# Optimization experiments

Hardware: AMD Instinct MI355X
Metric: run time of the kernel (lower is better)

## Reference

```python
import jax, jax.numpy as jnp
import numpy as np

HEADS = 16
HEAD_DIM = 64
EMB = 1024
B, S = 4, 2048
SCALE = 1.0 / 8.0  # fixed constant in the original code
MASK_PENALTY = -50.0  # original adds -50 * upper_triangular, not -inf


def setup_inputs() -> dict:
    key = jax.random.key(0)
    ks = jax.random.split(key, 5)
    x = jax.random.normal(ks[0], (B, S, EMB), dtype=jnp.float32)
    Wq = jax.random.normal(ks[1], (EMB, HEADS * HEAD_DIM), dtype=jnp.float32) * 0.02
    Wk = jax.random.normal(ks[2], (EMB, HEADS * HEAD_DIM), dtype=jnp.float32) * 0.02
    Wv = jax.random.normal(ks[3], (EMB, HEADS * HEAD_DIM), dtype=jnp.float32) * 0.02
    Wr = jax.random.normal(ks[4], (HEADS * HEAD_DIM, EMB), dtype=jnp.float32) * 0.02
    return {"x": x, "Wq": Wq, "Wk": Wk, "Wv": Wv, "Wr": Wr}


def reference(x, Wq, Wk, Wv, Wr):
    b, s, _ = x.shape
    # project and split heads: [b, s, h, d]
    q = (x @ Wq).reshape(b, s, HEADS, HEAD_DIM)
    k = (x @ Wk).reshape(b, s, HEADS, HEAD_DIM)
    v = (x @ Wv).reshape(b, s, HEADS, HEAD_DIM)
    # scores: [b, h, s, s]
    scores = SCALE * jnp.einsum('bqhd,bkhd->bhqk', q, k)
    # causal additive mask: -50 on strictly-upper triangle (faithful to original)
    causal = jnp.triu(jnp.ones((s, s), dtype=x.dtype), k=1)
    scores = scores + MASK_PENALTY * causal
    attn = jax.nn.softmax(scores, axis=-1)
    out = jnp.einsum('bhqk,bkhd->bqhd', attn, v).reshape(b, s, HEADS * HEAD_DIM)
    return out @ Wr
```

## Files before the change

kernel.cpp:

```cpp
#include <hip/hip_runtime.h>

typedef _Float16 f16;
typedef _Float16 f16x8 __attribute__((ext_vector_type(8)));
typedef _Float16 f16x4 __attribute__((ext_vector_type(4)));
typedef float f32x4 __attribute__((ext_vector_type(4)));
typedef float f32x16 __attribute__((ext_vector_type(16)));

#define MFMA16(A, B, C) __builtin_amdgcn_mfma_f32_16x16x32_f16((A), (B), (C), 0, 0, 0)
#define MFMA32(A, B, C) __builtin_amdgcn_mfma_f32_32x32x16_f16((A), (B), (C), 0, 0, 0)
#define MFMA16K16(A, B, C) __builtin_amdgcn_mfma_f32_16x16x16f16((A), (B), (C), 0, 0, 0)

__device__ __forceinline__ void async16(void* lds, const void* gp) {
    __builtin_amdgcn_global_load_lds(
        (__attribute__((address_space(1))) void*)(gp),
        (__attribute__((address_space(3))) void*)(lds), 16, 0, 0);
}

__global__ __launch_bounds__(256) void k_convert(const float* __restrict__ in,
                                                 f16* __restrict__ out, int n) {
    int i = (blockIdx.x * 256 + threadIdx.x) * 4;
    if (i + 3 < n) {
        float4 v = *(const float4*)(in + i);
        f16x4 o = {(f16)v.x, (f16)v.y, (f16)v.z, (f16)v.w};
        *(f16x4*)(out + i) = o;
    }
}

__global__ __launch_bounds__(256) void k_transpose_w4(const float* __restrict__ Wq,
                                                      const float* __restrict__ Wk,
                                                      const float* __restrict__ Wv,
                                                      const float* __restrict__ Wr,
                                                      f16* __restrict__ Wqkvt,
                                                      f16* __restrict__ Wrt) {
    __shared__ float tile[32][33];
    int z = blockIdx.z;
    const float* W = (z == 0) ? Wq : (z == 1) ? Wk : (z == 2) ? Wv : Wr;
    f16* Wt = (z == 3) ? Wrt : Wqkvt + z * 1048576;
    int c0 = blockIdx.x * 32, r0 = blockIdx.y * 32;
    int tx = threadIdx.x, ty = threadIdx.y;
#pragma unroll
    for (int j = 0; j < 32; j += 8)
        tile[ty + j][tx] = W[(r0 + ty + j) * 1024 + c0 + tx];
    __syncthreads();
#pragma unroll
    for (int j = 0; j < 32; j += 8)
        Wt[(c0 + ty + j) * 1024 + r0 + tx] = (f16)tile[tx][ty + j];
}

__global__ __launch_bounds__(256) void k_transpose_v(const f16* __restrict__ QKV,
                                                     f16* __restrict__ Vt) {
    __shared__ f16 tile[32][33];
    int s0 = blockIdx.x * 32;
    int d0 = blockIdx.y * 32;
    int bh = blockIdx.z;
    int b = bh >> 4, h = bh & 15;
    int tx = threadIdx.x, ty = threadIdx.y;
#pragma unroll
    for (int j = 0; j < 32; j += 8)
        tile[ty + j][tx] = QKV[(b * 2048 + s0 + ty + j) * 3072 + 2048 + h * 64 + d0 + tx];
    __syncthreads();
#pragma unroll
    for (int j = 0; j < 32; j += 8)
        Vt[(bh * 64 + d0 + ty + j) * 2048 + s0 + tx] = tile[tx][ty + j];
}

template <bool OUT_F16>
__global__ __launch_bounds__(256, 4) void k_gemm_bt(const f16* __restrict__ A,
                                                    const f16* __restrict__ Bt,
                                                    void* __restrict__ Cv,
                                                    int M, int N, int K) {
    __shared__ f16 As[128][32];
    __shared__ f16 Bs[128][32];
    int t = threadIdx.x;
    int lane = t & 63, w = t >> 6;
    int wm = (w >> 1) * 64, wn = (w & 1) * 64;
    int m0 = blockIdx.y * 128, n0 = blockIdx.x * 128;
    int ln = lane & 31, kh = lane >> 5;
    int sw = (ln >> 1) & 3;

    int lin0 = w * 128 + lane, lin1 = lin0 + 64;
    int r0 = lin0 >> 2, c0 = (lin0 & 3) ^ ((r0 >> 1) & 3);
    int r1 = lin1 >> 2, c1 = (lin1 & 3) ^ ((r1 >> 1) & 3);
    const f16* gA0 = A + (size_t)(m0 + r0) * K + c0 * 8;
    const f16* gA1 = A + (size_t)(m0 + r1) * K + c1 * 8;
    const f16* gB0 = Bt + (size_t)(n0 + r0) * K + c0 * 8;
    const f16* gB1 = Bt + (size_t)(n0 + r1) * K + c1 * 8;
    f16* lA0 = &As[0][0] + w * 1024;
    f16* lB0 = &Bs[0][0] + w * 1024;

    f32x16 acc[2][2] = {};

    for (int k0 = 0; k0 < K; k0 += 32) {
        __syncthreads();
        async16(lA0, gA0 + k0);
        async16(lA0 + 512, gA1 + k0);
        async16(lB0, gB0 + k0);
        async16(lB0 + 512, gB1 + k0);
        __syncthreads();
#pragma unroll
        for (int kd = 0; kd < 2; kd++) {
            int c = kd * 2 + kh;
            f16x8 af[2], bf[2];
#pragma unroll
            for (int mt = 0; mt < 2; mt++)
                af[mt] = *(const f16x8*)&As[wm + mt * 32 + ln][(c ^ sw) * 8];
#pragma unroll
            for (int nt = 0; nt < 2; nt++)
                bf[nt] = *(const f16x8*)&Bs[wn + nt * 32 + ln][(c ^ sw) * 8];
#pragma unroll
            for (int mt = 0; mt < 2; mt++)
#pragma unroll
                for (int nt = 0; nt < 2; nt++)
                    acc[mt][nt] = MFMA32(af[mt], bf[nt], acc[mt][nt]);
        }
    }

#pragma unroll
    for (int mt = 0; mt < 2; mt++)
#pragma unroll
        for (int nt = 0; nt < 2; nt++)
#pragma unroll
            for (int r = 0; r < 16; r++) {
                int row = m0 + wm + mt * 32 + (r & 3) + 8 * (r >> 2) + 4 * kh;
                int col = n0 + wn + nt * 32 + ln;
                float v = acc[mt][nt][r];
                if (OUT_F16)
                    ((f16*)Cv)[(size_t)row * N + col] = (f16)v;
                else
                    ((float*)Cv)[(size_t)row * N + col] = v;
            }
}

__global__ __launch_bounds__(256, 2) void k_attn(const f16* __restrict__ QKV,
                                                 const f16* __restrict__ Vt,
                                                 f16* __restrict__ Ob) {
    __shared__ f16 Ks[64][72];
    __shared__ f16 Vs[64][72];
    int bh = blockIdx.x;
    int y = blockIdx.y;
    int qt = (y < 4) ? (7 - y) : (y - 4);
    int b = bh >> 4, h = bh & 15;
    int q0 = qt * 256;
    int t = threadIdx.x, lane = t & 63, wq = t >> 6;
    int ln = lane & 15, g = lane >> 4, g8 = g * 8, rg = g * 4;
    int qw = q0 + wq * 64;

    int kr0 = t >> 3, kc0 = (t & 7) * 8;
    int kr1 = (t + 256) >> 3, kc1 = (t & 7) * 8;
    const f16* Kbase = QKV + (size_t)b * 2048 * 3072 + 1024 + h * 64;
    const f16* Vbase = Vt + (size_t)bh * 64 * 2048;

    const float C_SCL = 0.18033688f;
    const float C_MSK = -72.134752f;
    f16x4 ones4 = {(f16)1.f, (f16)1.f, (f16)1.f, (f16)1.f};

    f16x8 bq[4][2];
#pragma unroll
    for (int nt = 0; nt < 4; nt++)
#pragma unroll
        for (int kd = 0; kd < 2; kd++)
            bq[nt][kd] = *(const f16x8*)(QKV +
                (size_t)(b * 2048 + qw + nt * 16 + ln) * 3072 + h * 64 + kd * 32 + g8);

    int4 rk0 = *(const int4*)(Kbase + (size_t)kr0 * 3072 + kc0);
    int4 rk1 = *(const int4*)(Kbase + (size_t)kr1 * 3072 + kc1);
    int4 rv0 = *(const int4*)(Vbase + (size_t)kr0 * 2048 + kc0);
    int4 rv1 = *(const int4*)(Vbase + (size_t)kr1 * 2048 + kc1);

    f32x4 oacc[4][4] = {};
    f32x4 osum[4] = {};
    int nk = 4 * qt + 4;

    for (int kt = 0; kt < nk; kt++) {
        int k0 = kt * 64;
        __syncthreads();
        *(int4*)&Ks[kr0][kc0] = rk0;
        *(int4*)&Ks[kr1][kc1] = rk1;
        *(int4*)&Vs[kr0][kc0] = rv0;
        *(int4*)&Vs[kr1][kc1] = rv1;
        if (kt + 1 < nk) {
            int kn = k0 + 64;
            rk0 = *(const int4*)(Kbase + (size_t)(kn + kr0) * 3072 + kc0);
            rk1 = *(const int4*)(Kbase + (size_t)(kn + kr1) * 3072 + kc1);
            rv0 = *(const int4*)(Vbase + (size_t)kr0 * 2048 + kn + kc0);
            rv1 = *(const int4*)(Vbase + (size_t)kr1 * 2048 + kn + kc1);
        }
        __syncthreads();

        if (k0 > qw + 63) continue;

        f32x4 sacc[4][4] = {};
#pragma unroll
        for (int kd = 0; kd < 2; kd++) {
            f16x8 ak[4];
#pragma unroll
            for (int mt = 0; mt < 4; mt++)
                ak[mt] = *(const f16x8*)&Ks[mt * 16 + ln][kd * 32 + g8];
#pragma unroll
            for (int mt = 0; mt < 4; mt++)
#pragma unroll
                for (int nt = 0; nt < 4; nt++)
                    sacc[mt][nt] = MFMA16(ak[mt], bq[nt][kd], sacc[mt][nt]);
        }

        bool needs_mask = (k0 + 63 > qw);
        f16x4 pk[4][4];
#pragma unroll
        for (int nt = 0; nt < 4; nt++) {
            int q = qw + nt * 16 + ln;
#pragma unroll
            for (int mt = 0; mt < 4; mt++) {
#pragma unroll
                for (int r = 0; r < 4; r++) {
                    float e;
                    if (needs_mask) {
                        int kk = k0 + mt * 16 + rg + r;
                        e = __builtin_amdgcn_exp2f(
                            fmaf(sacc[mt][nt][r], C_SCL, (kk > q) ? C_MSK : 0.f));
                    } else {
                        e = __builtin_amdgcn_exp2f(sacc[mt][nt][r] * C_SCL);
                    }
                    pk[mt][nt][r] = (f16)e;
                }
            }
        }

#pragma unroll
        for (int mt = 0; mt < 4; mt++) {
            f16x4 bv[4];
#pragma unroll
            for (int dt = 0; dt < 4; dt++)
                bv[dt] = *(const f16x4*)&Vs[dt * 16 + ln][mt * 16 + rg];
#pragma unroll
            for (int nt = 0; nt < 4; nt++) {
#pragma unroll
                for (int dt = 0; dt < 4; dt++)
                    oacc[nt][dt] = MFMA16K16(pk[mt][nt], bv[dt], oacc[nt][dt]);
                osum[nt] = MFMA16K16(pk[mt][nt], ones4, osum[nt]);
            }
        }
    }

#pragma unroll
    for (int nt = 0; nt < 4; nt++)
#pragma unroll
        for (int r = 0; r < 4; r++) {
            float inv = __builtin_amdgcn_rcpf(osum[nt][r]);
            int row = b * 2048 + qw + nt * 16 + rg + r;
#pragma unroll
            for (int dt = 0; dt < 4; dt++)
                Ob[(size_t)row * 1024 + h * 64 + dt * 16 + ln] =
                    (f16)(oacc[nt][dt][r] * inv);
        }
}

extern "C" void kernel_launch(void* const* d_in, const int* in_sizes, int n_in,
                              void* d_out, int out_size, void* d_ws, size_t ws_size,
                              hipStream_t stream) {
    const float* x = (const float*)d_in[0];
    const float* Wq = (const float*)d_in[1];
    const float* Wk = (const float*)d_in[2];
    const float* Wv = (const float*)d_in[3];
    const float* Wr = (const float*)d_in[4];
    float* out = (float*)d_out;

    f16* ws = (f16*)d_ws;
    f16* xb    = ws;
    f16* Wqkvt = xb + 8388608;
    f16* Wrt   = Wqkvt + 3145728;
    f16* QKVb  = Wrt + 1048576;
    f16* Vtb   = QKVb + 25165824;
    f16* Obuf  = Vtb + 8388608;

    k_convert<<<8192, 256, 0, stream>>>(x, xb, 8388608);
    dim3 tb(32, 8);
    k_transpose_w4<<<dim3(32, 32, 4), tb, 0, stream>>>(Wq, Wk, Wv, Wr, Wqkvt, Wrt);
    k_gemm_bt<true><<<dim3(24, 64), 256, 0, stream>>>(xb, Wqkvt, QKVb, 8192, 3072, 1024);
    k_transpose_v<<<dim3(64, 2, 64), tb, 0, stream>>>(QKVb, Vtb);
    k_attn<<<dim3(64, 8), 256, 0, stream>>>(QKVb, Vtb, Obuf);
    k_gemm_bt<false><<<dim3(8, 64), 256, 0, stream>>>(Obuf, Wrt, out, 8192, 1024, 1024);
}
```

Measured before the change: 290.6 us.

## Split attention key range across blocks and pair query tiles with atomic merge

Each attention block now handles two query tiles, one long and one short causal range, which evens out work per block. It processes only half of each tile's key range and accumulates unnormalized outputs and row sums into fp32 buffers with atomicAdd. A new finalize kernel then normalizes and converts to fp16. The output buffer is reused as the accumulator. This adds two memsets, many global atomics and an extra pass over a 32 MB fp32 buffer, all to remove load imbalance and the tail from causal tiles of uneven length.

```diff
diff --git a/kernel.cpp b/kernel.cpp
--- a/kernel.cpp
+++ b/kernel.cpp
@@ -133,17 +133,15 @@
 
 __global__ __launch_bounds__(256, 2) void k_attn(const f16* __restrict__ QKV,
                                                  const f16* __restrict__ Vt,
-                                                 f16* __restrict__ Ob) {
+                                                 float* __restrict__ Oacc,
+                                                 float* __restrict__ Lacc) {
     __shared__ f16 Ks[64][72];
     __shared__ f16 Vs[64][72];
     int bh = blockIdx.x;
-    int y = blockIdx.y;
-    int qt = (y < 4) ? (7 - y) : (y - 4);
+    int p = blockIdx.y & 3, khalf = blockIdx.y >> 2;
     int b = bh >> 4, h = bh & 15;
-    int q0 = qt * 256;
     int t = threadIdx.x, lane = t & 63, wq = t >> 6;
     int ln = lane & 15, g = lane >> 4, g8 = g * 8, rg = g * 4;
-    int qw = q0 + wq * 64;
 
     int kr0 = t >> 3, kc0 = (t & 7) * 8;
     int kr1 = (t + 256) >> 3, kc1 = (t & 7) * 8;
@@ -154,104 +152,133 @@
     const float C_MSK = -72.134752f;
     f16x4 ones4 = {(f16)1.f, (f16)1.f, (f16)1.f, (f16)1.f};
 
-    f16x8 bq[4][2];
-#pragma unroll
-    for (int nt = 0; nt < 4; nt++)
-#pragma unroll
-        for (int kd = 0; kd < 2; kd++)
-            bq[nt][kd] = *(const f16x8*)(QKV +
-                (size_t)(b * 2048 + qw + nt * 16 + ln) * 3072 + h * 64 + kd * 32 + g8);
-
-    int4 rk0 = *(const int4*)(Kbase + (size_t)kr0 * 3072 + kc0);
-    int4 rk1 = *(const int4*)(Kbase + (size_t)kr1 * 3072 + kc1);
-    int4 rv0 = *(const int4*)(Vbase + (size_t)kr0 * 2048 + kc0);
-    int4 rv1 = *(const int4*)(Vbase + (size_t)kr1 * 2048 + kc1);
-
-    f32x4 oacc[4][4] = {};
-    f32x4 osum[4] = {};
-    int nk = 4 * qt + 4;
-
-    for (int kt = 0; kt < nk; kt++) {
-        int k0 = kt * 64;
-        __syncthreads();
-        *(int4*)&Ks[kr0][kc0] = rk0;
-        *(int4*)&Ks[kr1][kc1] = rk1;
-        *(int4*)&Vs[kr0][kc0] = rv0;
-        *(int4*)&Vs[kr1][kc1] = rv1;
-        if (kt + 1 < nk) {
-            int kn = k0 + 64;
-            rk0 = *(const int4*)(Kbase + (size_t)(kn + kr0) * 3072 + kc0);
-            rk1 = *(const int4*)(Kbase + (size_t)(kn + kr1) * 3072 + kc1);
-            rv0 = *(const int4*)(Vbase + (size_t)kr0 * 2048 + kn + kc0);
-            rv1 = *(const int4*)(Vbase + (size_t)kr1 * 2048 + kn + kc1);
+    int qtA = 7 - p, nkA = 4 * qtA + 4, cntA = nkA >> 1, sA = khalf * cntA;
+    int qtB = p,     nkB = 4 * qtB + 4, cntB = nkB >> 1, sB = khalf * cntB;
+
+    int4 rk0, rk1, rv0, rv1;
+    {
+        int kk = sA * 64;
+        rk0 = *(const int4*)(Kbase + (size_t)(kk + kr0) * 3072 + kc0);
+        rk1 = *(const int4*)(Kbase + (size_t)(kk + kr1) * 3072 + kc1);
+        rv0 = *(const int4*)(Vbase + (size_t)kr0 * 2048 + kk + kc0);
+        rv1 = *(const int4*)(Vbase + (size_t)kr1 * 2048 + kk + kc1);
+    }
+
+    for (int phase = 0; phase < 2; phase++) {
+        int qt = phase ? qtB : qtA;
+        int s = phase ? sB : sA;
+        int cnt = phase ? cntB : cntA;
+        int q0 = qt * 256;
+        int qw = q0 + wq * 64;
+
+        f16x8 bq[4][2];
+#pragma unroll
+        for (int nt = 0; nt < 4; nt++)
+#pragma unroll
+            for (int kd = 0; kd < 2; kd++)
+                bq[nt][kd] = *(const f16x8*)(QKV +
+                    (size_t)(b * 2048 + qw + nt * 16 + ln) * 3072 + h * 64 + kd * 32 + g8);
+
+        f32x4 oacc[4][4] = {};
+        f32x4 osum[4] = {};
+
+        for (int j = 0; j < cnt; j++) {
+            int k0 = (s + j) * 64;
+            __syncthreads();
+            *(int4*)&Ks[kr0][kc0] = rk0;
+            *(int4*)&Ks[kr1][kc1] = rk1;
+            *(int4*)&Vs[kr0][kc0] = rv0;
+            *(int4*)&Vs[kr1][kc1] = rv1;
+            int nxt = (j + 1 < cnt) ? (s + j + 1) : ((phase == 0) ? sB : -1);
+            if (nxt >= 0) {
+                int kk = nxt * 64;
+                rk0 = *(const int4*)(Kbase + (size_t)(kk + kr0) * 3072 + kc0);
+                rk1 = *(const int4*)(Kbase + (size_t)(kk + kr1) * 3072 + kc1);
+                rv0 = *(const int4*)(Vbase + (size_t)kr0 * 2048 + kk + kc0);
+                rv1 = *(const int4*)(Vbase + (size_t)kr1 * 2048 + kk + kc1);
+            }
+            __syncthreads();
+
+            if (k0 > qw + 63) continue;
+
+            f32x4 sacc[4][4] = {};
+#pragma unroll
+            for (int kd = 0; kd < 2; kd++) {
+                f16x8 ak[4];
+#pragma unroll
+                for (int mt = 0; mt < 4; mt++)
+                    ak[mt] = *(const f16x8*)&Ks[mt * 16 + ln][kd * 32 + g8];
+#pragma unroll
+                for (int mt = 0; mt < 4; mt++)
+#pragma unroll
+                    for (int nt = 0; nt < 4; nt++)
+                        sacc[mt][nt] = MFMA16(ak[mt], bq[nt][kd], sacc[mt][nt]);
+            }
+
+            bool needs_mask = (k0 + 63 > qw);
+            f16x4 pk[4][4];
+#pragma unroll
+            for (int nt = 0; nt < 4; nt++) {
+                int q = qw + nt * 16 + ln;
+#pragma unroll
+                for (int mt = 0; mt < 4; mt++) {
+#pragma unroll
+                    for (int r = 0; r < 4; r++) {
+                        float e;
+                        if (needs_mask) {
+                            int kk = k0 + mt * 16 + rg + r;
+                            e = __builtin_amdgcn_exp2f(
+                                fmaf(sacc[mt][nt][r], C_SCL, (kk > q) ? C_MSK : 0.f));
+                        } else {
+                            e = __builtin_amdgcn_exp2f(sacc[mt][nt][r] * C_SCL);
+                        }
+                        pk[mt][nt][r] = (f16)e;
+                    }
+                }
+            }
+
+#pragma unroll
+            for (int mt = 0; mt < 4; mt++) {
+                f16x4 bv[4];
+#pragma unroll
+                for (int dt = 0; dt < 4; dt++)
+                    bv[dt] = *(const f16x4*)&Vs[dt * 16 + ln][mt * 16 + rg];
+#pragma unroll
+                for (int nt = 0; nt < 4; nt++) {
+#pragma unroll
+                    for (int dt = 0; dt < 4; dt++)
+                        oacc[nt][dt] = MFMA16K16(pk[mt][nt], bv[dt], oacc[nt][dt]);
+                    osum[nt] = MFMA16K16(pk[mt][nt], ones4, osum[nt]);
+                }
+            }
         }
-        __syncthreads();
-
-        if (k0 > qw + 63) continue;
-
-        f32x4 sacc[4][4] = {};
-#pragma unroll
-        for (int kd = 0; kd < 2; kd++) {
-            f16x8 ak[4];
-#pragma unroll
-            for (int mt = 0; mt < 4; mt++)
-                ak[mt] = *(const f16x8*)&Ks[mt * 16 + ln][kd * 32 + g8];
-#pragma unroll
-            for (int mt = 0; mt < 4; mt++)
-#pragma unroll
-                for (int nt = 0; nt < 4; nt++)
-                    sacc[mt][nt] = MFMA16(ak[mt], bq[nt][kd], sacc[mt][nt]);
-        }
-
-        bool needs_mask = (k0 + 63 > qw);
-        f16x4 pk[4][4];
-#pragma unroll
-        for (int nt = 0; nt < 4; nt++) {
-            int q = qw + nt * 16 + ln;
-#pragma unroll
-            for (int mt = 0; mt < 4; mt++) {
-#pragma unroll
-                for (int r = 0; r < 4; r++) {
-                    float e;
-                    if (needs_mask) {
-                        int kk = k0 + mt * 16 + rg + r;
-                        e = __builtin_amdgcn_exp2f(
-                            fmaf(sacc[mt][nt][r], C_SCL, (kk > q) ? C_MSK : 0.f));
-                    } else {
-                        e = __builtin_amdgcn_exp2f(sacc[mt][nt][r] * C_SCL);
-                    }
-                    pk[mt][nt][r] = (f16)e;
-                }
-            }
-        }
-
-#pragma unroll
-        for (int mt = 0; mt < 4; mt++) {
-            f16x4 bv[4];
-#pragma unroll
-            for (int dt = 0; dt < 4; dt++)
-                bv[dt] = *(const f16x4*)&Vs[dt * 16 + ln][mt * 16 + rg];
-#pragma unroll
-            for (int nt = 0; nt < 4; nt++) {
+
+#pragma unroll
+        for (int nt = 0; nt < 4; nt++)
+#pragma unroll
+            for (int r = 0; r < 4; r++) {
+                int q = qw + nt * 16 + rg + r;
+                size_t row = (size_t)(b * 2048 + q);
 #pragma unroll
                 for (int dt = 0; dt < 4; dt++)
-                    oacc[nt][dt] = MFMA16K16(pk[mt][nt], bv[dt], oacc[nt][dt]);
-                osum[nt] = MFMA16K16(pk[mt][nt], ones4, osum[nt]);
-            }
-        }
+                    atomicAdd(&Oacc[row * 1024 + h * 64 + dt * 16 + ln],
+                              oacc[nt][dt][r]);
+                if (ln == 0)
+                    atomicAdd(&Lacc[(size_t)bh * 2048 + q], osum[nt][r]);
+            }
     }
-
-#pragma unroll
-    for (int nt = 0; nt < 4; nt++)
-#pragma unroll
-        for (int r = 0; r < 4; r++) {
-            float inv = __builtin_amdgcn_rcpf(osum[nt][r]);
-            int row = b * 2048 + qw + nt * 16 + rg + r;
-#pragma unroll
-            for (int dt = 0; dt < 4; dt++)
-                Ob[(size_t)row * 1024 + h * 64 + dt * 16 + ln] =
-                    (f16)(oacc[nt][dt][r] * inv);
-        }
+}
+
+__global__ __launch_bounds__(256) void k_finalize(const float* __restrict__ Oacc,
+                                                  const float* __restrict__ Lacc,
+                                                  f16* __restrict__ Ob) {
+    int i = (blockIdx.x * 256 + threadIdx.x) * 4;
+    int row = i >> 10, col = i & 1023;
+    int b = row >> 11, q = row & 2047, h = col >> 6;
+    float inv = __builtin_amdgcn_rcpf(Lacc[(size_t)(b * 16 + h) * 2048 + q]);
+    float4 v = *(const float4*)(Oacc + i);
+    f16x4 o = {(f16)(v.x * inv), (f16)(v.y * inv), (f16)(v.z * inv), (f16)(v.w * inv)};
+    *(f16x4*)(Ob + i) = o;
 }
 
 extern "C" void kernel_launch(void* const* d_in, const int* in_sizes, int n_in,
@@ -271,12 +298,17 @@
     f16* QKVb  = Wrt + 1048576;
     f16* Vtb   = QKVb + 25165824;
     f16* Obuf  = Vtb + 8388608;
+    float* Lacc = (float*)(Obuf + 8388608);
+    float* Oacc = out;
 
     k_convert<<<8192, 256, 0, stream>>>(x, xb, 8388608);
     dim3 tb(32, 8);
     k_transpose_w4<<<dim3(32, 32, 4), tb, 0, stream>>>(Wq, Wk, Wv, Wr, Wqkvt, Wrt);
     k_gemm_bt<true><<<dim3(24, 64), 256, 0, stream>>>(xb, Wqkvt, QKVb, 8192, 3072, 1024);
     k_transpose_v<<<dim3(64, 2, 64), tb, 0, stream>>>(QKVb, Vtb);
-    k_attn<<<dim3(64, 8), 256, 0, stream>>>(QKVb, Vtb, Obuf);
+    hipMemsetAsync(Oacc, 0, (size_t)8388608 * 4, stream);
+    hipMemsetAsync(Lacc, 0, (size_t)131072 * 4, stream);
+    k_attn<<<dim3(64, 8), 256, 0, stream>>>(QKVb, Vtb, Oacc, Lacc);
+    k_finalize<<<8192, 256, 0, stream>>>(Oacc, Lacc, Obuf);
     k_gemm_bt<false><<<dim3(8, 64), 256, 0, stream>>>(Obuf, Wrt, out, 8192, 1024, 1024);
 }
```

Result: slower. 321.9 us (+10.8%).
